# Kernel optimization log

Measured on AMD Instinct MI355X. Metric: run time of the kernel, lower is better.

Reference implementation:

```python
import jax, jax.numpy as jnp
import numpy as np

B, N, D, A = 256, 32, 128, 16
DOA, E, FD, H, O = 144, 128, 128, 256, 1  # obs_act_in, obs_out/embed, final_in, hidden, final_out


def setup_inputs() -> dict:
    key = jax.random.key(0)
    ks = jax.random.split(key, 12)
    p = lambda k, shape: jax.random.normal(k, shape, jnp.float32) * 0.05
    return {
        "states": jax.random.normal(ks[0], (B, N, D), jnp.float32),
        "policies": jax.random.uniform(ks[1], (B, N, A), dtype=jnp.float32),
        "actions": jax.random.uniform(ks[2], (B, N, A), dtype=jnp.float32),
        "Wk_proc": p(ks[3], (D, E)),
        "Wq_proc": p(ks[4], (D, E)),
        "Wv_proc": p(ks[5], (D, E)),
        "Wk": p(ks[6], (E, FD)),
        "Wq": p(ks[7], (E, FD)),
        "We": p(ks[8], (DOA, E)),
        "Wav": p(ks[9], (E, FD)),
        "W1": p(ks[10], (FD, H)),
        "W2": p(ks[11], (H, O)),
    }


def reference(states, policies, actions, Wk_proc, Wq_proc, Wv_proc, Wk, Wq, We, Wav, W1, W2):
    n = states.shape[1]
    # NOTE: original code divides BOTH attention stages by sqrt(self.d_k_obs) = final_input_dim
    scale = 1.0 / jnp.sqrt(jnp.asarray(Wk.shape[1], states.dtype))

    # stage-1 attention over agents [B,N,N]
    k1 = states @ Wk_proc
    q1 = states @ Wq_proc
    v1 = states @ Wv_proc
    w1 = jax.nn.softmax(jnp.einsum('bie,bje->bij', q1, k1) * scale, axis=-1)
    wav1 = jnp.einsum('bij,bje->bie', w1, v1)  # [B,N,E]

    # stage-2 attention weights
    k2 = wav1 @ Wk
    q2 = wav1 @ Wq
    w2 = jax.nn.softmax(jnp.einsum('bif,bjf->bij', q2, k2) * scale, axis=-1)

    # build obs-action/policy tensor: entry [b,i,j] uses policy of agent j when i==j else action of j
    oa = jnp.concatenate([states, actions], axis=-1)   # [B,N,DOA]
    op = jnp.concatenate([states, policies], axis=-1)  # [B,N,DOA]
    eye = jnp.eye(n, dtype=states.dtype)[:, :, None]   # [N,N,1]
    oap = eye * op[:, None, :, :] + (1.0 - eye) * oa[:, None, :, :]  # [B,N,N,DOA]

    av = (oap @ We) @ Wav  # [B,N,N,FD]

    # node_features[b,i,j,f] = sum_k w2[b,i,k] * av[b,j,k,f]  (avoids the 5D repeat)
    node = jnp.einsum('bik,bjkf->bijf', w2, av)

    h = node @ W1
    h = jnp.where(h > 0, h, 0.01 * h)  # leaky_relu, default slope
    value = h @ W2  # [B,N,N,O]
    return value, w1, w2
```

## Files before the change

### kernel.cpp

```cpp
#include <hip/hip_runtime.h>
#include <math.h>

#define NB 256
#define NN 32
#define DD 128
#define NA 16
#define HH 256

using f32x4v  = __attribute__((ext_vector_type(4))) float;
using bf16x8  = __attribute__((ext_vector_type(8))) short;

static __device__ __forceinline__ float4 ld4(const float* p){ return *reinterpret_cast<const float4*>(p); }
static __device__ __forceinline__ void st4f(float* p, float4 v){ *reinterpret_cast<float4*>(p) = v; }
static __device__ __forceinline__ float elem(float4 v, int kk){
    return (kk==0)?v.x:(kk==1)?v.y:(kk==2)?v.z:v.w;
}

static __device__ __forceinline__ unsigned f2bf(float x){
    unsigned u = __float_as_uint(x);
    u += 0x7fffu + ((u >> 16) & 1u);
    return u >> 16;
}
static __device__ __forceinline__ unsigned pack2(float a, float b){
    return f2bf(a) | (f2bf(b) << 16);
}
static __device__ __forceinline__ float bf2f(unsigned short s){
    return __uint_as_float(((unsigned)s) << 16);
}

static __device__ __forceinline__ f32x4v mfma16(bf16x8 a, bf16x8 b, f32x4v c){
    return __builtin_amdgcn_mfma_f32_16x16x32_bf16(a, b, c, 0, 0, 0);
}

static __device__ __forceinline__ void store_frag(unsigned short* __restrict__ dst,
                                                  int frag, int l, const float v[8]){
    uint4 p;
    p.x = pack2(v[0], v[1]); p.y = pack2(v[2], v[3]);
    p.z = pack2(v[4], v[5]); p.w = pack2(v[6], v[7]);
    *reinterpret_cast<uint4*>(dst + (size_t)(frag*64 + l)*8) = p;
}

__global__ __launch_bounds__(512)
void k_pre(const float* __restrict__ We, const float* __restrict__ Wav,
           const float* __restrict__ W1,
           const float* __restrict__ Wqp, const float* __restrict__ Wkp,
           const float* __restrict__ Wvp, const float* __restrict__ Wq,
           const float* __restrict__ Wk,
           float* __restrict__ WABf, unsigned short* __restrict__ WABs,
           unsigned short* __restrict__ Wqps, unsigned short* __restrict__ Wkps,
           unsigned short* __restrict__ Wvps, unsigned short* __restrict__ Wqs,
           unsigned short* __restrict__ Wks)
{
    __shared__ float W1c[128*16];
    __shared__ float WABt[160*16];
    const int t = threadIdx.x;
    const int bid = blockIdx.x;

    if (bid < 16) {
        const int ct = bid;

        {
            int k = t >> 2, c4 = (t & 3) * 4;
            st4f(W1c + k*16 + c4, ld4(W1 + k*256 + ct*16 + c4));
        }
        __syncthreads();

        const int m = t >> 2, cq = t & 3;
        float a1[4] = {0.f,0.f,0.f,0.f};
        {
            const float* wrow = Wav + m*128;
            #pragma unroll 4
            for (int k0 = 0; k0 < 128; k0 += 4) {
                float4 xv = ld4(wrow + k0);
                #pragma unroll
                for (int kk = 0; kk < 4; kk++) {
                    float4 wr = ld4(W1c + (k0+kk)*16 + cq*4);
                    float x = elem(xv, kk);
                    a1[0] = fmaf(x, wr.x, a1[0]);
                    a1[1] = fmaf(x, wr.y, a1[1]);
                    a1[2] = fmaf(x, wr.z, a1[2]);
                    a1[3] = fmaf(x, wr.w, a1[3]);
                }
            }
        }
        __syncthreads();
        st4f(W1c + m*16 + cq*4, make_float4(a1[0],a1[1],a1[2],a1[3]));
        __syncthreads();

        const int rg = t >> 4, c = t & 15;
        const bool v4 = (rg < 16);
        float a2[5] = {0.f,0.f,0.f,0.f,0.f};
        {
            #pragma unroll 2
            for (int k0 = 0; k0 < 128; k0 += 4) {
                float4 xv[5];
                #pragma unroll
                for (int u = 0; u < 4; u++) xv[u] = ld4(We + (rg + 32*u)*128 + k0);
                xv[4] = v4 ? ld4(We + (128 + rg)*128 + k0) : make_float4(0.f,0.f,0.f,0.f);
                #pragma unroll
                for (int kk = 0; kk < 4; kk++) {
                    float w = W1c[(k0+kk)*16 + c];
                    #pragma unroll
                    for (int u = 0; u < 5; u++)
                        a2[u] = fmaf(elem(xv[u],kk), w, a2[u]);
                }
            }
        }
        #pragma unroll
        for (int u = 0; u < 5; u++)
            WABt[(rg + 32*u)*16 + c] = a2[u];
        if (v4) WABf[(size_t)(128 + rg)*256 + ct*16 + c] = a2[4];
        __syncthreads();

        if (t < 320) {
            int kt = t >> 6, l = t & 63;
            float v[8];
            #pragma unroll
            for (int i = 0; i < 8; i++)
                v[i] = WABt[(kt*32 + (l>>4)*8 + i)*16 + (l&15)];
            store_frag(WABs, kt*16 + ct, l, v);
        }
    } else {
        const int sel = (bid - 16) >> 1, half = (bid - 16) & 1;
        const float* W = (sel==0) ? Wqp : (sel==1) ? Wkp : (sel==2) ? Wvp :
                         (sel==3) ? Wq : Wk;
        unsigned short* dst = (sel==0) ? Wqps : (sel==1) ? Wkps : (sel==2) ? Wvps :
                              (sel==3) ? Wqs : Wks;
        #pragma unroll
        for (int ss = 0; ss < 2; ss++){
            int s = half*1024 + t + 512*ss;
            int frag = s >> 6, l = s & 63;
            int kt = frag >> 3, nt = frag & 7;
            float v[8];
            #pragma unroll
            for (int i=0;i<8;i++)
                v[i] = W[(kt*32 + (l>>4)*8 + i)*128 + nt*16 + (l&15)];
            store_frag(dst, frag, l, v);
        }
    }
}

static __device__ __forceinline__ void scores_softmax512(const float* __restrict__ Qm,
                                                         const float* __restrict__ Km,
                                                         float scale,
                                                         float* __restrict__ w_lds,
                                                         float* __restrict__ w_out,
                                                         int i, int j)
{
    float s0 = 0.f, s1 = 0.f;
    #pragma unroll 4
    for (int k=0;k<128;k+=4){
        float4 qv = ld4(Qm + i*132 + k);
        float4 k0 = ld4(Km + j*132 + k);
        float4 k1 = ld4(Km + (j+16)*132 + k);
        s0 += qv.x*k0.x + qv.y*k0.y + qv.z*k0.z + qv.w*k0.w;
        s1 += qv.x*k1.x + qv.y*k1.y + qv.z*k1.z + qv.w*k1.w;
    }
    s0 *= scale; s1 *= scale;
    float m = fmaxf(s0, s1);
    #pragma unroll
    for (int d=1; d<16; d<<=1) m = fmaxf(m, __shfl_xor(m, d));
    float e0 = expf(s0 - m), e1 = expf(s1 - m);
    float sum = e0 + e1;
    #pragma unroll
    for (int d=1; d<16; d<<=1) sum += __shfl_xor(sum, d);
    float inv = 1.f / sum;
    e0 *= inv; e1 *= inv;
    w_lds[i*36 + j]      = e0;
    w_lds[i*36 + j + 16] = e1;
    w_out[i*32 + j]      = e0;
    w_out[i*32 + j + 16] = e1;
}

__global__ __launch_bounds__(512)
void k_main(const float* __restrict__ states, const float* __restrict__ pol,
            const float* __restrict__ act,
            const unsigned short* __restrict__ Wqps, const unsigned short* __restrict__ Wkps,
            const unsigned short* __restrict__ Wvps, const unsigned short* __restrict__ Wqs,
            const unsigned short* __restrict__ Wks,  const unsigned short* __restrict__ WABs,
            const float* __restrict__ WABf, const float* __restrict__ W2,
            float* __restrict__ out_v, float* __restrict__ out_w1,
            float* __restrict__ out_w2)
{
    const int b = blockIdx.x;
    const int t = threadIdx.x;
    const float scale = 0.08838834764831845f;

    __shared__ float SH[16000];
    float* B1   = SH;
    float* B2   = SH + 4224;
    float* Wb2f = SH + 8448;
    float* Wb1f = SH + 9600;
    float* APd  = SH + 10752;
    unsigned short* Xoa  = (unsigned short*)(SH + 11264);
    unsigned short* Ubf  = (unsigned short*)B1;
    unsigned short* Wvbf = (unsigned short*)B2;
    float*    A1 = SH;
    unsigned* P2 = (unsigned*)(SH + 11904);
    unsigned* Q2 = (unsigned*)SH;

    const float* stg  = states + (size_t)b*(NN*DD);
    const float* actg = act + (size_t)b*(NN*NA);
    const float* polg = pol + (size_t)b*(NN*NA);

    {
        int r = t >> 4, kb = t & 15;
        #pragma unroll
        for (int uu = 0; uu < 10; uu++){
            int k = kb + 16*uu;
            float v = (k < 128) ? stg[r*128 + k]
                    : (k < 144) ? actg[r*16 + (k-128)] : 0.f;
            Xoa[r*168 + k] = (unsigned short)f2bf(v);
        }
        if (t < 128) {
            int rr = t>>2, cc = (t&3)*4;
            float4 p = ld4(polg + rr*16 + cc), a = ld4(actg + rr*16 + cc);
            st4f(APd + rr*16 + cc, make_float4(p.x-a.x, p.y-a.y, p.z-a.z, p.w-a.w));
        }
    }
    __syncthreads();

    const int l    = t & 63;
    const int wv   = t >> 6;
    const int mt   = wv & 1;
    const int ntb  = (wv >> 1) * 2;
    const int arow = mt*16 + (l & 15);
    const int drow = mt*16 + ((l >> 4) << 2);
    const int dcol = l & 15;

    const int c  = t & 127;
    const int g  = t >> 7;
    const int cp = (t & 127)*2;
    const int si = t >> 4;
    const int sj = t & 15;

    {
        f32x4v aq0={0.f,0.f,0.f,0.f}, aq1={0.f,0.f,0.f,0.f};
        f32x4v ak0={0.f,0.f,0.f,0.f}, ak1={0.f,0.f,0.f,0.f};
        const unsigned short* ab = Xoa + arow*168 + (l>>4)*8;
        #pragma unroll
        for (int kt = 0; kt < 4; kt++){
            bf16x8 a   = *reinterpret_cast<const bf16x8*>(ab + kt*32);
            bf16x8 bq0 = *reinterpret_cast<const bf16x8*>(Wqps + (size_t)((kt*8+ntb  )*64 + l)*8);
            bf16x8 bq1 = *reinterpret_cast<const bf16x8*>(Wqps + (size_t)((kt*8+ntb+1)*64 + l)*8);
            bf16x8 bk0 = *reinterpret_cast<const bf16x8*>(Wkps + (size_t)((kt*8+ntb  )*64 + l)*8);
            bf16x8 bk1 = *reinterpret_cast<const bf16x8*>(Wkps + (size_t)((kt*8+ntb+1)*64 + l)*8);
            aq0 = mfma16(a, bq0, aq0); aq1 = mfma16(a, bq1, aq1);
            ak0 = mfma16(a, bk0, ak0); ak1 = mfma16(a, bk1, ak1);
        }
        #pragma unroll
        for (int r = 0; r < 4; r++){
            B1[(drow+r)*132 + ntb*16     + dcol] = aq0[r];
            B1[(drow+r)*132 + (ntb+1)*16 + dcol] = aq1[r];
            B2[(drow+r)*132 + ntb*16     + dcol] = ak0[r];
            B2[(drow+r)*132 + (ntb+1)*16 + dcol] = ak1[r];
        }
    }
    __syncthreads();

    scores_softmax512(B1, B2, scale, Wb1f, out_w1 + (size_t)b*1024, si, sj);
    __syncthreads();

    {
        float au[8];
        #pragma unroll
        for (int u=0;u<8;u++) au[u]=0.f;
        #pragma unroll
        for (int k0=0;k0<32;k0+=4){
            float4 xv[8];
            #pragma unroll
            for (int u=0;u<8;u++) xv[u] = ld4(Wb1f + (g*8+u)*36 + k0);
            #pragma unroll
            for (int kk=0;kk<4;kk++){
                float w = bf2f(Xoa[(k0+kk)*168 + c]);
                #pragma unroll
                for (int u=0;u<8;u++) au[u] = fmaf(elem(xv[u],kk), w, au[u]);
            }
        }
        __syncthreads();
        #pragma unroll
        for (int u=0;u<8;u++) Ubf[(g*8+u)*136 + c] = (unsigned short)f2bf(au[u]);
    }
    __syncthreads();

    {
        f32x4v av0={0.f,0.f,0.f,0.f}, av1={0.f,0.f,0.f,0.f};
        const unsigned short* ab = Ubf + arow*136 + (l>>4)*8;
        #pragma unroll
        for (int kt = 0; kt < 4; kt++){
            bf16x8 a  = *reinterpret_cast<const bf16x8*>(ab + kt*32);
            bf16x8 b0 = *reinterpret_cast<const bf16x8*>(Wvps + (size_t)((kt*8+ntb  )*64 + l)*8);
            bf16x8 b1 = *reinterpret_cast<const bf16x8*>(Wvps + (size_t)((kt*8+ntb+1)*64 + l)*8);
            av0 = mfma16(a, b0, av0); av1 = mfma16(a, b1, av1);
        }
        #pragma unroll
        for (int r = 0; r < 4; r++){
            Wvbf[(drow+r)*136 + ntb*16     + dcol] = (unsigned short)f2bf(av0[r]);
            Wvbf[(drow+r)*136 + (ntb+1)*16 + dcol] = (unsigned short)f2bf(av1[r]);
        }
    }
    __syncthreads();

    {
        f32x4v aq0={0.f,0.f,0.f,0.f}, aq1={0.f,0.f,0.f,0.f};
        f32x4v ak0={0.f,0.f,0.f,0.f}, ak1={0.f,0.f,0.f,0.f};
        const unsigned short* ab = Wvbf + arow*136 + (l>>4)*8;
        #pragma unroll
        for (int kt = 0; kt < 4; kt++){
            bf16x8 a   = *reinterpret_cast<const bf16x8*>(ab + kt*32);
            bf16x8 bq0 = *reinterpret_cast<const bf16x8*>(Wqs + (size_t)((kt*8+ntb  )*64 + l)*8);
            bf16x8 bq1 = *reinterpret_cast<const bf16x8*>(Wqs + (size_t)((kt*8+ntb+1)*64 + l)*8);
            bf16x8 bk0 = *reinterpret_cast<const bf16x8*>(Wks + (size_t)((kt*8+ntb  )*64 + l)*8);
            bf16x8 bk1 = *reinterpret_cast<const bf16x8*>(Wks + (size_t)((kt*8+ntb+1)*64 + l)*8);
            aq0 = mfma16(a, bq0, aq0); aq1 = mfma16(a, bq1, aq1);
            ak0 = mfma16(a, bk0, ak0); ak1 = mfma16(a, bk1, ak1);
        }
        __syncthreads();
        #pragma unroll
        for (int r = 0; r < 4; r++){
            B1[(drow+r)*132 + ntb*16     + dcol] = aq0[r];
            B1[(drow+r)*132 + (ntb+1)*16 + dcol] = aq1[r];
            B2[(drow+r)*132 + ntb*16     + dcol] = ak0[r];
            B2[(drow+r)*132 + (ntb+1)*16 + dcol] = ak1[r];
        }
    }
    __syncthreads();

    scores_softmax512(B1, B2, scale, Wb2f, out_w2 + (size_t)b*1024, si, sj);
    __syncthreads();

    {
        f32x4v ac[4];
        #pragma unroll
        for (int n=0;n<4;n++) ac[n] = f32x4v{0.f,0.f,0.f,0.f};
        const int nb7 = (wv >> 1) * 4;
        const unsigned short* ab = Xoa + arow*168 + (l>>4)*8;
        #pragma unroll
        for (int kt = 0; kt < 5; kt++){
            bf16x8 a = *reinterpret_cast<const bf16x8*>(ab + kt*32);
            #pragma unroll
            for (int n = 0; n < 4; n++){
                bf16x8 bb = *reinterpret_cast<const bf16x8*>(WABs + (size_t)((kt*16 + nb7 + n)*64 + l)*8);
                ac[n] = mfma16(a, bb, ac[n]);
            }
        }
        #pragma unroll
        for (int n = 0; n < 4; n++){
            #pragma unroll
            for (int r = 0; r < 4; r++)
                A1[(drow+r)*260 + (nb7+n)*16 + dcol] = ac[n][r];
        }
    }
    __syncthreads();

    {
        float ap0[8], ap1[8];
        #pragma unroll
        for (int u=0;u<8;u++){ ap0[u]=0.f; ap1[u]=0.f; }
        #pragma unroll
        for (int k0=0;k0<32;k0+=4){
            float4 xv[8];
            #pragma unroll
            for (int u=0;u<8;u++) xv[u] = ld4(Wb2f + (g*8+u)*36 + k0);
            #pragma unroll
            for (int kk=0;kk<4;kk++){
                float2 w = *reinterpret_cast<const float2*>(A1 + (k0+kk)*260 + cp);
                #pragma unroll
                for (int u=0;u<8;u++){
                    float x = elem(xv[u],kk);
                    ap0[u] = fmaf(x, w.x, ap0[u]);
                    ap1[u] = fmaf(x, w.y, ap1[u]);
                }
            }
        }
        __syncthreads();
        #pragma unroll
        for (int u=0;u<8;u++)
            P2[(g*8+u)*128 + (cp>>1)] = pack2(ap0[u], ap1[u]);
    }
    __syncthreads();

    {
        float aq0[8], aq1[8];
        #pragma unroll
        for (int u=0;u<8;u++){ aq0[u]=0.f; aq1[u]=0.f; }
        const float* wB = WABf + 128*256;
        #pragma unroll
        for (int k0=0;k0<16;k0+=4){
            float4 xv[8];
            #pragma unroll
            for (int u=0;u<8;u++) xv[u] = ld4(APd + (g*8+u)*16 + k0);
            #pragma unroll
            for (int kk=0;kk<4;kk++){
                float2 w = *reinterpret_cast<const float2*>(wB + (k0+kk)*256 + cp);
                #pragma unroll
                for (int u=0;u<8;u++){
                    float x = elem(xv[u],kk);
                    aq0[u] = fmaf(x, w.x, aq0[u]);
                    aq1[u] = fmaf(x, w.y, aq1[u]);
                }
            }
        }
        #pragma unroll
        for (int u=0;u<8;u++)
            Q2[(g*8+u)*130 + (cp>>1)] = pack2(aq0[u], aq1[u]);
    }
    __syncthreads();

    {
        float w00 = Wb2f[si*36 + sj], w01 = Wb2f[si*36 + sj + 16];
        float a0 = 0.f, a1 = 0.f;

        #define STEP(P_, Q_, W_, W2H, ACC) {                       \
            float t_ = fmaf((W_), (Q_), (P_));                     \
            float u_ = fmaf(0.495f, fabsf(t_), 0.505f * t_);       \
            (ACC) = fmaf(u_, (W2H), (ACC)); }

        #pragma unroll 8
        for (int hp=0; hp<128; hp++){
            unsigned pa = P2[si*128 + hp];
            unsigned qa = Q2[sj*130 + hp];
            unsigned qb = Q2[(sj+16)*130 + hp];
            float w2e = W2[2*hp], w2o = W2[2*hp+1];
            float paE = __uint_as_float(pa<<16), paO = __uint_as_float(pa & 0xffff0000u);
            float qaE = __uint_as_float(qa<<16), qaO = __uint_as_float(qa & 0xffff0000u);
            float qbE = __uint_as_float(qb<<16), qbO = __uint_as_float(qb & 0xffff0000u);
            STEP(paE, qaE, w00, w2e, a0)  STEP(paO, qaO, w00, w2o, a0)
            STEP(paE, qbE, w01, w2e, a1)  STEP(paO, qbO, w01, w2o, a1)
        }
        #undef STEP

        float* ov = out_v + (size_t)b*1024;
        ov[si*32 + sj]      = a0;
        ov[si*32 + sj + 16] = a1;
    }
}

extern "C" void kernel_launch(void* const* d_in, const int* in_sizes, int n_in,
                              void* d_out, int out_size, void* d_ws, size_t ws_size,
                              hipStream_t stream) {
    const float* states = (const float*)d_in[0];
    const float* pol    = (const float*)d_in[1];
    const float* act    = (const float*)d_in[2];
    const float* Wkp    = (const float*)d_in[3];
    const float* Wqp    = (const float*)d_in[4];
    const float* Wvp    = (const float*)d_in[5];
    const float* Wk     = (const float*)d_in[6];
    const float* Wq     = (const float*)d_in[7];
    const float* We     = (const float*)d_in[8];
    const float* Wav    = (const float*)d_in[9];
    const float* W1     = (const float*)d_in[10];
    const float* W2     = (const float*)d_in[11];

    float* out    = (float*)d_out;
    float* out_v  = out;
    float* out_w1 = out + 256*1024;
    float* out_w2 = out + 2*256*1024;

    float* WABf = (float*)d_ws;
    unsigned short* WABs = (unsigned short*)(WABf + 36864);
    unsigned short* wsu  = (unsigned short*)(WABf + 57344);
    unsigned short* Wqps = wsu;
    unsigned short* Wkps = wsu + 16384;
    unsigned short* Wvps = wsu + 32768;
    unsigned short* Wqs  = wsu + 49152;
    unsigned short* Wks  = wsu + 65536;

    hipLaunchKernelGGL(k_pre, dim3(26), dim3(512), 0, stream,
                       We, Wav, W1, Wqp, Wkp, Wvp, Wq, Wk,
                       WABf, WABs, Wqps, Wkps, Wvps, Wqs, Wks);
    hipLaunchKernelGGL(k_main, dim3(NB), dim3(512), 0, stream,
                       states, pol, act,
                       Wqps, Wkps, Wvps, Wqs, Wks, WABs, WABf, W2,
                       out_v, out_w1, out_w2);
}
```

Baseline: 45.09 us.

## Split leaky-relu into linear plus abs terms and hoist work earlier

The final value loop now accumulates only |t|*W2 terms, since leaky_relu(t) = 0.505*t + 0.495*|t|. The linear part is precomputed as per-row reductions (SP, SQ) via wave shuffles, which saves a multiply per step in the inner loop. The loop also reads P2/Q2 as uint4 vectors, with Q2 padding changed to 132. The Q-projection and the oap MFMA are moved earlier to overlap with other stages, which removes some barriers, and k_pre now runs 1024 threads per block. The cost is higher register pressure from keeping qr/ac live across phases, plus extra shuffle reductions.

After: 44.97 us. Within noise of the previous version (-0.3%).

```diff
diff --git a/kernel.cpp b/kernel.cpp
--- a/kernel.cpp
+++ b/kernel.cpp
@@ -40,7 +40,7 @@
     *reinterpret_cast<uint4*>(dst + (size_t)(frag*64 + l)*8) = p;
 }
 
-__global__ __launch_bounds__(512)
+__global__ __launch_bounds__(1024)
 void k_pre(const float* __restrict__ We, const float* __restrict__ Wav,
            const float* __restrict__ W1,
            const float* __restrict__ Wqp, const float* __restrict__ Wkp,
@@ -60,13 +60,14 @@
         const int ct = bid;
 
         {
-            int k = t >> 2, c4 = (t & 3) * 4;
-            st4f(W1c + k*16 + c4, ld4(W1 + k*256 + ct*16 + c4));
+            int k = t >> 3, c2 = (t & 7) * 2;
+            *reinterpret_cast<float2*>(W1c + k*16 + c2) =
+                *reinterpret_cast<const float2*>(W1 + k*256 + ct*16 + c2);
         }
         __syncthreads();
 
-        const int m = t >> 2, cq = t & 3;
-        float a1[4] = {0.f,0.f,0.f,0.f};
+        const int m = t >> 3, cq2 = (t & 7) * 2;
+        float a1x = 0.f, a1y = 0.f;
         {
             const float* wrow = Wav + m*128;
             #pragma unroll 4
@@ -74,42 +75,40 @@
                 float4 xv = ld4(wrow + k0);
                 #pragma unroll
                 for (int kk = 0; kk < 4; kk++) {
-                    float4 wr = ld4(W1c + (k0+kk)*16 + cq*4);
+                    float2 wr = *reinterpret_cast<const float2*>(W1c + (k0+kk)*16 + cq2);
                     float x = elem(xv, kk);
-                    a1[0] = fmaf(x, wr.x, a1[0]);
-                    a1[1] = fmaf(x, wr.y, a1[1]);
-                    a1[2] = fmaf(x, wr.z, a1[2]);
-                    a1[3] = fmaf(x, wr.w, a1[3]);
+                    a1x = fmaf(x, wr.x, a1x);
+                    a1y = fmaf(x, wr.y, a1y);
                 }
             }
         }
         __syncthreads();
-        st4f(W1c + m*16 + cq*4, make_float4(a1[0],a1[1],a1[2],a1[3]));
+        W1c[m*16 + cq2]     = a1x;
+        W1c[m*16 + cq2 + 1] = a1y;
         __syncthreads();
 
         const int rg = t >> 4, c = t & 15;
-        const bool v4 = (rg < 16);
-        float a2[5] = {0.f,0.f,0.f,0.f,0.f};
+        float a20 = 0.f, a21 = 0.f, a22 = 0.f;
         {
             #pragma unroll 2
             for (int k0 = 0; k0 < 128; k0 += 4) {
-                float4 xv[5];
-                #pragma unroll
-                for (int u = 0; u < 4; u++) xv[u] = ld4(We + (rg + 32*u)*128 + k0);
-                xv[4] = v4 ? ld4(We + (128 + rg)*128 + k0) : make_float4(0.f,0.f,0.f,0.f);
+                float4 xv0 = ld4(We + rg*128 + k0);
+                float4 xv1 = ld4(We + (rg+64)*128 + k0);
+                float4 xv2 = (rg < 16) ? ld4(We + (128+rg)*128 + k0)
+                                       : make_float4(0.f,0.f,0.f,0.f);
                 #pragma unroll
                 for (int kk = 0; kk < 4; kk++) {
                     float w = W1c[(k0+kk)*16 + c];
-                    #pragma unroll
-                    for (int u = 0; u < 5; u++)
-                        a2[u] = fmaf(elem(xv[u],kk), w, a2[u]);
+                    a20 = fmaf(elem(xv0,kk), w, a20);
+                    a21 = fmaf(elem(xv1,kk), w, a21);
+                    a22 = fmaf(elem(xv2,kk), w, a22);
                 }
             }
         }
-        #pragma unroll
-        for (int u = 0; u < 5; u++)
-            WABt[(rg + 32*u)*16 + c] = a2[u];
-        if (v4) WABf[(size_t)(128 + rg)*256 + ct*16 + c] = a2[4];
+        WABt[rg*16 + c]      = a20;
+        WABt[(rg+64)*16 + c] = a21;
+        if (rg < 32) WABt[(128+rg)*16 + c] = a22;
+        if (rg < 16) WABf[(size_t)(128 + rg)*256 + ct*16 + c] = a22;
         __syncthreads();
 
         if (t < 320) {
@@ -126,17 +125,14 @@
                          (sel==3) ? Wq : Wk;
         unsigned short* dst = (sel==0) ? Wqps : (sel==1) ? Wkps : (sel==2) ? Wvps :
                               (sel==3) ? Wqs : Wks;
-        #pragma unroll
-        for (int ss = 0; ss < 2; ss++){
-            int s = half*1024 + t + 512*ss;
-            int frag = s >> 6, l = s & 63;
-            int kt = frag >> 3, nt = frag & 7;
-            float v[8];
-            #pragma unroll
-            for (int i=0;i<8;i++)
-                v[i] = W[(kt*32 + (l>>4)*8 + i)*128 + nt*16 + (l&15)];
-            store_frag(dst, frag, l, v);
-        }
+        int s = half*1024 + t;
+        int frag = s >> 6, l = s & 63;
+        int kt = frag >> 3, nt = frag & 7;
+        float v[8];
+        #pragma unroll
+        for (int i=0;i<8;i++)
+            v[i] = W[(kt*32 + (l>>4)*8 + i)*128 + nt*16 + (l&15)];
+        store_frag(dst, frag, l, v);
     }
 }
 
@@ -198,6 +194,7 @@
     float*    A1 = SH;
     unsigned* P2 = (unsigned*)(SH + 11904);
     unsigned* Q2 = (unsigned*)SH;
+    float* SPQ = Wb1f;
 
     const float* stg  = states + (size_t)b*(NN*DD);
     const float* actg = act + (size_t)b*(NN*NA);
@@ -224,6 +221,7 @@
     const int wv   = t >> 6;
     const int mt   = wv & 1;
     const int ntb  = (wv >> 1) * 2;
+    const int nb7  = (wv >> 1) * 4;
     const int arow = mt*16 + (l & 15);
     const int drow = mt*16 + ((l >> 4) << 2);
     const int dcol = l & 15;
@@ -233,6 +231,38 @@
     const int cp = (t & 127)*2;
     const int si = t >> 4;
     const int sj = t & 15;
+    const int wp = wv & 1;
+
+    float qr0[8], qr1[8], sq[8];
+    {
+        #pragma unroll
+        for (int u=0;u<8;u++){ qr0[u]=0.f; qr1[u]=0.f; }
+        const float* wB = WABf + 128*256;
+        #pragma unroll
+        for (int k0=0;k0<16;k0+=4){
+            float4 xv[8];
+            #pragma unroll
+            for (int u=0;u<8;u++) xv[u] = ld4(APd + (g*8+u)*16 + k0);
+            #pragma unroll
+            for (int kk=0;kk<4;kk++){
+                float2 w = *reinterpret_cast<const float2*>(wB + (k0+kk)*256 + cp);
+                #pragma unroll
+                for (int u=0;u<8;u++){
+                    float x = elem(xv[u],kk);
+                    qr0[u] = fmaf(x, w.x, qr0[u]);
+                    qr1[u] = fmaf(x, w.y, qr1[u]);
+                }
+            }
+        }
+        float2 w2v = *reinterpret_cast<const float2*>(W2 + cp);
+        #pragma unroll
+        for (int u=0;u<8;u++) sq[u] = qr0[u]*w2v.x + qr1[u]*w2v.y;
+        #pragma unroll
+        for (int d=1; d<64; d<<=1){
+            #pragma unroll
+            for (int u=0;u<8;u++) sq[u] += __shfl_xor(sq[u], d);
+        }
+    }
 
     {
         f32x4v aq0={0.f,0.f,0.f,0.f}, aq1={0.f,0.f,0.f,0.f};
@@ -256,6 +286,22 @@
             B2[(drow+r)*132 + (ntb+1)*16 + dcol] = ak1[r];
         }
     }
+
+    f32x4v ac[4];
+    {
+        #pragma unroll
+        for (int n=0;n<4;n++) ac[n] = f32x4v{0.f,0.f,0.f,0.f};
+        const unsigned short* ab = Xoa + arow*168 + (l>>4)*8;
+        #pragma unroll
+        for (int kt = 0; kt < 5; kt++){
+            bf16x8 a = *reinterpret_cast<const bf16x8*>(ab + kt*32);
+            #pragma unroll
+            for (int n = 0; n < 4; n++){
+                bf16x8 bb = *reinterpret_cast<const bf16x8*>(WABs + (size_t)((kt*16 + nb7 + n)*64 + l)*8);
+                ac[n] = mfma16(a, bb, ac[n]);
+            }
+        }
+    }
     __syncthreads();
 
     scores_softmax512(B1, B2, scale, Wb1f, out_w1 + (size_t)b*1024, si, sj);
@@ -277,7 +323,6 @@
                 for (int u=0;u<8;u++) au[u] = fmaf(elem(xv[u],kk), w, au[u]);
             }
         }
-        __syncthreads();
         #pragma unroll
         for (int u=0;u<8;u++) Ubf[(g*8+u)*136 + c] = (unsigned short)f2bf(au[u]);
     }
@@ -330,20 +375,6 @@
     __syncthreads();
 
     {
-        f32x4v ac[4];
-        #pragma unroll
-        for (int n=0;n<4;n++) ac[n] = f32x4v{0.f,0.f,0.f,0.f};
-        const int nb7 = (wv >> 1) * 4;
-        const unsigned short* ab = Xoa + arow*168 + (l>>4)*8;
-        #pragma unroll
-        for (int kt = 0; kt < 5; kt++){
-            bf16x8 a = *reinterpret_cast<const bf16x8*>(ab + kt*32);
-            #pragma unroll
-            for (int n = 0; n < 4; n++){
-                bf16x8 bb = *reinterpret_cast<const bf16x8*>(WABs + (size_t)((kt*16 + nb7 + n)*64 + l)*8);
-                ac[n] = mfma16(a, bb, ac[n]);
-            }
-        }
         #pragma unroll
         for (int n = 0; n < 4; n++){
             #pragma unroll
@@ -373,66 +404,68 @@
                 }
             }
         }
-        __syncthreads();
         #pragma unroll
         for (int u=0;u<8;u++)
             P2[(g*8+u)*128 + (cp>>1)] = pack2(ap0[u], ap1[u]);
-    }
-    __syncthreads();
-
-    {
-        float aq0[8], aq1[8];
-        #pragma unroll
-        for (int u=0;u<8;u++){ aq0[u]=0.f; aq1[u]=0.f; }
-        const float* wB = WABf + 128*256;
-        #pragma unroll
-        for (int k0=0;k0<16;k0+=4){
-            float4 xv[8];
-            #pragma unroll
-            for (int u=0;u<8;u++) xv[u] = ld4(APd + (g*8+u)*16 + k0);
-            #pragma unroll
-            for (int kk=0;kk<4;kk++){
-                float2 w = *reinterpret_cast<const float2*>(wB + (k0+kk)*256 + cp);
-                #pragma unroll
-                for (int u=0;u<8;u++){
-                    float x = elem(xv[u],kk);
-                    aq0[u] = fmaf(x, w.x, aq0[u]);
-                    aq1[u] = fmaf(x, w.y, aq1[u]);
-                }
-            }
-        }
+        float2 w2v = *reinterpret_cast<const float2*>(W2 + cp);
+        float sp[8];
+        #pragma unroll
+        for (int u=0;u<8;u++) sp[u] = ap0[u]*w2v.x + ap1[u]*w2v.y;
+        #pragma unroll
+        for (int d=1; d<64; d<<=1){
+            #pragma unroll
+            for (int u=0;u<8;u++) sp[u] += __shfl_xor(sp[u], d);
+        }
+        if (l == 0){
+            #pragma unroll
+            for (int u=0;u<8;u++) SPQ[(g*8+u)*2 + wp] = sp[u];
+        }
+    }
+    __syncthreads();
+
+    {
         #pragma unroll
         for (int u=0;u<8;u++)
-            Q2[(g*8+u)*130 + (cp>>1)] = pack2(aq0[u], aq1[u]);
+            Q2[(g*8+u)*132 + (cp>>1)] = pack2(qr0[u], qr1[u]);
+        if (l == 0){
+            #pragma unroll
+            for (int u=0;u<8;u++) SPQ[64 + (g*8+u)*2 + wp] = sq[u];
+        }
     }
     __syncthreads();
 
     {
         float w00 = Wb2f[si*36 + sj], w01 = Wb2f[si*36 + sj + 16];
+        float SPi = SPQ[si*2] + SPQ[si*2+1];
+        float SQa = SPQ[64 + sj*2] + SPQ[64 + sj*2+1];
+        float SQb = SPQ[64 + (sj+16)*2] + SPQ[64 + (sj+16)*2+1];
         float a0 = 0.f, a1 = 0.f;
 
-        #define STEP(P_, Q_, W_, W2H, ACC) {                       \
-            float t_ = fmaf((W_), (Q_), (P_));                     \
-            float u_ = fmaf(0.495f, fabsf(t_), 0.505f * t_);       \
-            (ACC) = fmaf(u_, (W2H), (ACC)); }
-
-        #pragma unroll 8
-        for (int hp=0; hp<128; hp++){
-            unsigned pa = P2[si*128 + hp];
-            unsigned qa = Q2[sj*130 + hp];
-            unsigned qb = Q2[(sj+16)*130 + hp];
-            float w2e = W2[2*hp], w2o = W2[2*hp+1];
-            float paE = __uint_as_float(pa<<16), paO = __uint_as_float(pa & 0xffff0000u);
-            float qaE = __uint_as_float(qa<<16), qaO = __uint_as_float(qa & 0xffff0000u);
-            float qbE = __uint_as_float(qb<<16), qbO = __uint_as_float(qb & 0xffff0000u);
-            STEP(paE, qaE, w00, w2e, a0)  STEP(paO, qaO, w00, w2o, a0)
-            STEP(paE, qbE, w01, w2e, a1)  STEP(paO, qbO, w01, w2o, a1)
-        }
-        #undef STEP
+        #define PROC(PA,QA,QB,H2) {                                         \
+            float w2e = W2[(H2)], w2o = W2[(H2)+1];                         \
+            float paE = __uint_as_float((PA)<<16), paO = __uint_as_float((PA) & 0xffff0000u); \
+            float qaE = __uint_as_float((QA)<<16), qaO = __uint_as_float((QA) & 0xffff0000u); \
+            float qbE = __uint_as_float((QB)<<16), qbO = __uint_as_float((QB) & 0xffff0000u); \
+            float t0 = fmaf(w00, qaE, paE); a0 = fmaf(fabsf(t0), w2e, a0);  \
+            float t1 = fmaf(w00, qaO, paO); a0 = fmaf(fabsf(t1), w2o, a0);  \
+            float t2 = fmaf(w01, qbE, paE); a1 = fmaf(fabsf(t2), w2e, a1);  \
+            float t3 = fmaf(w01, qbO, paO); a1 = fmaf(fabsf(t3), w2o, a1); }
+
+        #pragma unroll 4
+        for (int hp4 = 0; hp4 < 32; hp4++){
+            uint4 pa4 = *reinterpret_cast<const uint4*>(P2 + si*128 + hp4*4);
+            uint4 qa4 = *reinterpret_cast<const uint4*>(Q2 + sj*132 + hp4*4);
+            uint4 qb4 = *reinterpret_cast<const uint4*>(Q2 + (sj+16)*132 + hp4*4);
+            PROC(pa4.x, qa4.x, qb4.x, hp4*8+0)
+            PROC(pa4.y, qa4.y, qb4.y, hp4*8+2)
+            PROC(pa4.z, qa4.z, qb4.z, hp4*8+4)
+            PROC(pa4.w, qa4.w, qb4.w, hp4*8+6)
+        }
+        #undef PROC
 
         float* ov = out_v + (size_t)b*1024;
-        ov[si*32 + sj]      = a0;
-        ov[si*32 + sj + 16] = a1;
+        ov[si*32 + sj]      = fmaf(0.495f, a0, 0.505f*(SPi + w00*SQa));
+        ov[si*32 + sj + 16] = fmaf(0.495f, a1, 0.505f*(SPi + w01*SQb));
     }
 }
 
@@ -466,7 +499,7 @@
     unsigned short* Wqs  = wsu + 49152;
     unsigned short* Wks  = wsu + 65536;
 
-    hipLaunchKernelGGL(k_pre, dim3(26), dim3(512), 0, stream,
+    hipLaunchKernelGGL(k_pre, dim3(26), dim3(1024), 0, stream,
                        We, Wav, W1, Wqp, Wkp, Wvp, Wq, Wk,
                        WABf, WABs, Wqps, Wkps, Wvps, Wqs, Wks);
     hipLaunchKernelGGL(k_main, dim3(NB), dim3(512), 0, stream,
```
